# Kernel optimization log

Measured on AMD Instinct MI355X. Metric: run time of the kernel, lower is better.

Reference implementation:

```python
import jax, jax.numpy as jnp
import numpy as np

N = 50000
E = 800000
T = 12
HID = 128
K = 3
F_IN = 7  # 1 (x) + 4 (env) + 2 (coords)
CIN = F_IN + HID  # DCRNN concatenates input with hidden state


def setup_inputs() -> dict:
    key = jax.random.key(0)
    ks = jax.random.split(key, 16)
    inp = {
        "x": jax.random.normal(ks[0], (N, T), dtype=jnp.float32),
        "env": jax.random.normal(ks[1], (N, 4, T), dtype=jnp.float32),
        "coords": jax.random.uniform(ks[2], (N, 2), dtype=jnp.float32),
        "edge_index": jax.random.randint(ks[3], (2, E), 0, N, dtype=jnp.int32),
        "edge_weight": jax.random.uniform(ks[4], (E,), dtype=jnp.float32),
        "local_night": jax.random.uniform(ks[5], (N, T + 1), dtype=jnp.float32),
        # DCRNN gate diffusion-conv weights: [2 (out/in direction), K, Cin, Cout]
        "Wz": jax.random.normal(ks[6], (2, K, CIN, HID), dtype=jnp.float32) * 0.05,
        "bz": jnp.zeros((HID,), dtype=jnp.float32),
        "Wr": jax.random.normal(ks[7], (2, K, CIN, HID), dtype=jnp.float32) * 0.05,
        "br": jnp.zeros((HID,), dtype=jnp.float32),
        "Wh": jax.random.normal(ks[8], (2, K, CIN, HID), dtype=jnp.float32) * 0.05,
        "bh": jnp.zeros((HID,), dtype=jnp.float32),
        "lin_W": jax.random.normal(ks[9], (HID, 1), dtype=jnp.float32) * 0.05,
        "lin_b": jnp.zeros((1,), dtype=jnp.float32),
    }
    return inp


def reference(x, env, coords, edge_weight, local_night, Wz, bz, Wr, br, Wh, bh, lin_W, lin_b, edge_index):
    row, col = edge_index[0], edge_index[1]
    n = x.shape[0]

    # out/in degrees of the weighted adjacency A[row, col] = w
    deg_out = jax.ops.segment_sum(edge_weight, row, num_segments=n)
    deg_in = jax.ops.segment_sum(edge_weight, col, num_segments=n)
    inv_out = jnp.where(deg_out > 0, 1.0 / deg_out, 0.0)
    inv_in = jnp.where(deg_in > 0, 1.0 / deg_in, 0.0)

    def prop_out(v):  # (D_O^{-1} A) v : gather from col, scatter-add to row
        msg = edge_weight[:, None] * v[col]
        return inv_out[:, None] * jax.ops.segment_sum(msg, row, num_segments=n)

    def prop_in(v):  # (D_I^{-1} A^T) v : gather from row, scatter-add to col
        msg = edge_weight[:, None] * v[row]
        return inv_in[:, None] * jax.ops.segment_sum(msg, col, num_segments=n)

    def dconv(X, W, b):
        # K-hop bidirectional diffusion convolution
        H = X @ (W[0, 0] + W[1, 0])
        Tx0 = X
        Tx_o = prop_out(X)
        Tx_i = prop_in(X)
        H = H + Tx_o @ W[0, 1] + Tx_i @ W[1, 1]
        for k in range(2, W.shape[1]):
            Tx_o = 2.0 * prop_out(Tx_o) - Tx0
            Tx_i = 2.0 * prop_in(Tx_i) - Tx0
            H = H + Tx_o @ W[0, k] + Tx_i @ W[1, k]
        return H + b

    env_t = jnp.moveaxis(env, -1, 0)          # [T, N, 4]
    night_t = jnp.transpose(local_night[:, 1:])  # [T, N]
    hid0 = jnp.zeros((n, HID), dtype=x.dtype)   # hidden state resets each call (H=None)

    def step(x_prev, ts):
        e, night = ts
        X = jnp.concatenate([x_prev, e, coords], axis=1)   # [N, 7]
        Xh = jnp.concatenate([X, hid0], axis=1)            # [N, 7+HID]
        Z = jax.nn.sigmoid(dconv(Xh, Wz, bz))
        R = jax.nn.sigmoid(dconv(Xh, Wr, br))  # H*R = 0 since H0 = 0; kept for fidelity
        H_tilde = jnp.tanh(dconv(Xh, Wh, bh))
        H_new = Z * hid0 + (1.0 - Z) * H_tilde
        out = jax.nn.relu(H_new) @ lin_W + lin_b           # [N, 1]
        out = out * night[:, None]
        return out, out

    x0 = x[:, 0:1]
    _, preds = jax.lax.scan(step, x0, (env_t, night_t))    # preds: [T, N, 1]
    predictions = jnp.concatenate([x0, jnp.transpose(preds[..., 0])], axis=1)  # [N, T+1]
    return predictions
```

## Files before the change

kernel.cpp:

```cpp
#include <hip/hip_runtime.h>
#include <hip/hip_fp16.h>

#define Nn 50000
#define Ee 800000
#define Tt 12
#define NBAND 8
#define BAND 6250
#define CAP 64

__global__ __launch_bounds__(256) void csr_direct(
    const int* __restrict__ ei, const float* __restrict__ ew,
    int* __restrict__ nextR, int* __restrict__ nextC,
    unsigned* __restrict__ adjR, unsigned* __restrict__ adjC)
{
    int band = blockIdx.x & (NBAND - 1);
    int chunk = blockIdx.x >> 3;
    int lo = band * BAND, hi = lo + BAND;
    int stride = (gridDim.x >> 3) * 256;
    for (int e = chunk * 256 + threadIdx.x; e < Ee; e += stride) {
        int r = ei[e], c = ei[Ee + e];
        bool br = (r >= lo) & (r < hi);
        bool bc = (c >= lo) & (c < hi);
        if (br | bc) {
            unsigned wb = __half_as_ushort(__float2half(ew[e]));
            if (br) adjR[(r << 6) + atomicAdd(&nextR[r], 1)] = ((unsigned)c << 16) | wb;
            if (bc) adjC[(c << 6) + atomicAdd(&nextC[c], 1)] = ((unsigned)r << 16) | wb;
        }
    }
}

__global__ __launch_bounds__(256) void weff_kernel(
    const float* __restrict__ Wz, const float* __restrict__ Wh,
    const float* __restrict__ bz, const float* __restrict__ bh,
    float* __restrict__ wzT, float* __restrict__ whT)
{
    int idx = blockIdx.x * 256 + threadIdx.x;
    if (idx >= 2 * 36 * 128) return;
    const float* W = (idx < 36 * 128) ? Wz : Wh;
    const float* B = (idx < 36 * 128) ? bz : bh;
    float* O       = (idx < 36 * 128) ? wzT : whT;
    int rem = idx % (36 * 128);
    int k = rem / 128, j = rem % 128;
    float v;
    if (k == 35) v = B[j];
    else {
        int p = k / 7, rr = k % 7;
        if (p == 0)      v = W[(0 * 135 + rr) * 128 + j] + W[(3 * 135 + rr) * 128 + j];
        else if (p == 1) v = W[(1 * 135 + rr) * 128 + j];
        else if (p == 2) v = W[(4 * 135 + rr) * 128 + j];
        else if (p == 3) v = W[(2 * 135 + rr) * 128 + j];
        else             v = W[(5 * 135 + rr) * 128 + j];
    }
    O[k * 128 + j] = v;
}

__global__ __launch_bounds__(256) void initS_kernel(
    const float* __restrict__ x, const float* __restrict__ env,
    const float* __restrict__ coords,
    __half* __restrict__ S, __half* __restrict__ xcur, float* __restrict__ out)
{
    int i = blockIdx.x * 256 + threadIdx.x;
    if (i >= Nn) return;
    float xv = x[i * Tt];
    xcur[i] = __float2half(xv);
    out[i * 13] = xv;
    float4 ev[12];
    const float4* ep = (const float4*)(env + (long)i * 48);
    #pragma unroll
    for (int j = 0; j < 12; j++) ev[j] = ep[j];
    const float* evf = (const float*)ev;
    __half row[64];
    #pragma unroll
    for (int t = 0; t < 12; t++)
        #pragma unroll
        for (int c = 0; c < 4; c++)
            row[t * 4 + c] = __float2half(evf[c * 12 + t]);
    row[48] = __float2half(coords[i * 2]);
    row[49] = __float2half(coords[i * 2 + 1]);
    #pragma unroll
    for (int j = 50; j < 64; j++) row[j] = __half(0.f);
    uint4* dst = (uint4*)(S + (long)i * 64);
    const uint4* sv = (const uint4*)row;
    #pragma unroll
    for (int j = 0; j < 8; j++) dst[j] = sv[j];
}

__device__ __forceinline__ float wdec(unsigned ed) {
    return __half2float(__ushort_as_half((unsigned short)(ed & 0xffffu)));
}

__device__ __forceinline__ void acc8h(float* a, float w, uint4 hv) {
    float2 p0 = __half22float2(*(__half2*)&hv.x);
    float2 p1 = __half22float2(*(__half2*)&hv.y);
    float2 p2 = __half22float2(*(__half2*)&hv.z);
    float2 p3 = __half22float2(*(__half2*)&hv.w);
    a[0] = fmaf(w, p0.x, a[0]); a[1] = fmaf(w, p0.y, a[1]);
    a[2] = fmaf(w, p1.x, a[2]); a[3] = fmaf(w, p1.y, a[3]);
    a[4] = fmaf(w, p2.x, a[4]); a[5] = fmaf(w, p2.y, a[5]);
    a[6] = fmaf(w, p3.x, a[6]); a[7] = fmaf(w, p3.y, a[7]);
}

__device__ __forceinline__ void unpack8h(uint4 hv, float* f) {
    float2 p0 = __half22float2(*(__half2*)&hv.x);
    float2 p1 = __half22float2(*(__half2*)&hv.y);
    float2 p2 = __half22float2(*(__half2*)&hv.z);
    float2 p3 = __half22float2(*(__half2*)&hv.w);
    f[0] = p0.x; f[1] = p0.y; f[2] = p1.x; f[3] = p1.y;
    f[4] = p2.x; f[5] = p2.y; f[6] = p3.x; f[7] = p3.y;
}

__global__ __launch_bounds__(256) void prop_kernel(
    const int* __restrict__ cntR, const unsigned* __restrict__ adjR,
    const int* __restrict__ cntC, const unsigned* __restrict__ adjC,
    const __half* __restrict__ src_o, const __half* __restrict__ src_i,
    const __half* __restrict__ subS,
    __half* __restrict__ dst_o, __half* __restrict__ dst_i,
    float* __restrict__ inv_out, float* __restrict__ inv_in, int computeInv)
{
    int tid = blockIdx.x * 256 + threadIdx.x;
    if (tid >= Nn * 16) return;
    int team = tid >> 3;
    int node = team >> 1, dir = team & 1, s = tid & 7;
    const int*      cn  = dir ? cntC : cntR;
    const unsigned* adj = dir ? adjC : adjR;
    const __half*   src = dir ? src_i : src_o;
    __half*         dst = dir ? dst_i : dst_o;
    int b = node << 6, e = b + cn[node];
    float acc[8] = {0.f,0.f,0.f,0.f,0.f,0.f,0.f,0.f};
    float sw = 0.f;
    for (int k = b; k < e; k += 4) {
        bool v1 = k + 1 < e, v2 = k + 2 < e, v3 = k + 3 < e;
        unsigned e0 = adj[k];
        unsigned e1 = adj[v1 ? k + 1 : b];
        unsigned e2 = adj[v2 ? k + 2 : b];
        unsigned e3 = adj[v3 ? k + 3 : b];
        uint4 r0 = *(const uint4*)(src + (long)(e0 >> 16) * 64 + s * 8);
        uint4 r1 = *(const uint4*)(src + (long)(e1 >> 16) * 64 + s * 8);
        uint4 r2 = *(const uint4*)(src + (long)(e2 >> 16) * 64 + s * 8);
        uint4 r3 = *(const uint4*)(src + (long)(e3 >> 16) * 64 + s * 8);
        float w0 = wdec(e0);
        float w1 = v1 ? wdec(e1) : 0.f;
        float w2 = v2 ? wdec(e2) : 0.f;
        float w3 = v3 ? wdec(e3) : 0.f;
        acc8h(acc, w0, r0); acc8h(acc, w1, r1);
        acc8h(acc, w2, r2); acc8h(acc, w3, r3);
        sw += (w0 + w1) + (w2 + w3);
    }
    float inv;
    if (computeInv) {
        inv = sw > 0.f ? 1.f / sw : 0.f;
        if (s == 0) (dir ? inv_in : inv_out)[node] = inv;
    } else {
        inv = (dir ? inv_in : inv_out)[node];
    }
    float o8[8];
    if (subS) {
        uint4 sv4 = *(const uint4*)(subS + (long)node * 64 + s * 8);
        float sv[8];
        unpack8h(sv4, sv);
        #pragma unroll
        for (int q = 0; q < 8; q++) o8[q] = fmaf(2.f * inv, acc[q], -sv[q]);
    } else {
        #pragma unroll
        for (int q = 0; q < 8; q++) o8[q] = inv * acc[q];
    }
    __half2 h0 = __floats2half2_rn(o8[0], o8[1]);
    __half2 h1 = __floats2half2_rn(o8[2], o8[3]);
    __half2 h2 = __floats2half2_rn(o8[4], o8[5]);
    __half2 h3 = __floats2half2_rn(o8[6], o8[7]);
    uint4 st;
    st.x = *(unsigned*)&h0; st.y = *(unsigned*)&h1;
    st.z = *(unsigned*)&h2; st.w = *(unsigned*)&h3;
    *(uint4*)(dst + (long)node * 64 + s * 8) = st;
}

__global__ __launch_bounds__(256) void gx_kernel(
    const int* __restrict__ cntR, const unsigned* __restrict__ adjR,
    const int* __restrict__ cntC, const unsigned* __restrict__ adjC,
    const __half* __restrict__ xcur,
    __half* __restrict__ toX, __half* __restrict__ tiX,
    const float* __restrict__ inv_out, const float* __restrict__ inv_in)
{
    int tid = blockIdx.x * 256 + threadIdx.x;
    if (tid >= Nn * 8) return;
    int node = tid >> 3;
    int dir = (tid >> 2) & 1, sub = tid & 3;
    const int*      cn  = dir ? cntC : cntR;
    const unsigned* adj = dir ? adjC : adjR;
    int b = node << 6, e = b + cn[node];
    float acc = 0.f;
    int k0 = b + sub;
    {
        unsigned en[6]; bool v[6];
        #pragma unroll
        for (int s = 0; s < 6; s++) { int k = k0 + 4 * s; v[s] = k < e; en[s] = adj[v[s] ? k : b]; }
        __half xv[6];
        #pragma unroll
        for (int s = 0; s < 6; s++) xv[s] = xcur[v[s] ? (en[s] >> 16) : 0u];
        #pragma unroll
        for (int s = 0; s < 6; s++) acc += (v[s] ? wdec(en[s]) : 0.f) * __half2float(xv[s]);
        for (int k = k0 + 24; k < e; k += 4) {
            unsigned ed = adj[k];
            acc += wdec(ed) * __half2float(xcur[ed >> 16]);
        }
    }
    acc += __shfl_xor(acc, 1);
    acc += __shfl_xor(acc, 2);
    if (sub == 0) {
        float inv = (dir ? inv_in : inv_out)[node];
        (dir ? tiX : toX)[node] = __float2half(inv * acc);
    }
}

__global__ __launch_bounds__(256) void step_kernel(
    const int* __restrict__ cntR, const unsigned* __restrict__ adjR,
    const int* __restrict__ cntC, const unsigned* __restrict__ adjC,
    const float* __restrict__ inv_out, const float* __restrict__ inv_in,
    const float* __restrict__ env, const float* __restrict__ coords,
    const float* __restrict__ night,
    const float* __restrict__ wzT, const float* __restrict__ whT,
    const float* __restrict__ linW, const float* __restrict__ linb,
    __half* __restrict__ xcur,
    const __half* __restrict__ toX, const __half* __restrict__ tiX,
    const __half* __restrict__ P_o, const __half* __restrict__ P_i,
    const __half* __restrict__ P2_o, const __half* __restrict__ P2_i,
    float* __restrict__ out, int t)
{
    __shared__ float f_s[32][36];
    __shared__ float part_s[2][32];
    int tid = threadIdx.x;
    int base = blockIdx.x * 32;

    {
        int nl = tid >> 3;
        int dir = (tid >> 2) & 1, sub = tid & 3;
        int node = base + nl;
        int nc = node < Nn ? node : Nn - 1;
        const int*      cn  = dir ? cntC : cntR;
        const unsigned* adj = dir ? adjC : adjR;
        const __half*   src = dir ? tiX : toX;
        int b = nc << 6, e = b + cn[nc];
        float acc = 0.f;
        int k0 = b + sub;
        {
            unsigned en[6]; bool v[6];
            #pragma unroll
            for (int s = 0; s < 6; s++) { int k = k0 + 4 * s; v[s] = k < e; en[s] = adj[v[s] ? k : b]; }
            __half xv[6];
            #pragma unroll
            for (int s = 0; s < 6; s++) xv[s] = src[v[s] ? (en[s] >> 16) : 0u];
            #pragma unroll
            for (int s = 0; s < 6; s++) acc += (v[s] ? wdec(en[s]) : 0.f) * __half2float(xv[s]);
            for (int k = k0 + 24; k < e; k += 4) {
                unsigned ed = adj[k];
                acc += wdec(ed) * __half2float(src[ed >> 16]);
            }
        }
        acc += __shfl_xor(acc, 1);
        acc += __shfl_xor(acc, 2);
        if (sub == 0) {
            float inv = (dir ? inv_in : inv_out)[nc];
            float xval = __half2float(xcur[nc]);
            f_s[nl][21 + 7 * dir] = fmaf(2.f * inv, acc, -xval);
        }
    }
    {
        int g = tid >> 5;
        int n = tid & 31;
        int node = base + n;
        int nc = node < Nn ? node : Nn - 1;
        if (g == 0) {
            f_s[n][0] = __half2float(xcur[nc]);
            #pragma unroll
            for (int c = 0; c < 4; c++) f_s[n][1 + c] = env[(long)nc * 48 + c * 12 + t];
            f_s[n][5] = coords[nc * 2];
            f_s[n][6] = coords[nc * 2 + 1];
            f_s[n][35] = 1.f;
        } else if (g == 1) {
            f_s[n][7] = __half2float(toX[nc]);
            const __half* r = P_o + (long)nc * 64;
            #pragma unroll
            for (int c = 0; c < 4; c++) f_s[n][8 + c] = __half2float(r[t * 4 + c]);
            f_s[n][12] = __half2float(r[48]);
            f_s[n][13] = __half2float(r[49]);
        } else if (g == 2) {
            f_s[n][14] = __half2float(tiX[nc]);
            const __half* r = P_i + (long)nc * 64;
            #pragma unroll
            for (int c = 0; c < 4; c++) f_s[n][15 + c] = __half2float(r[t * 4 + c]);
            f_s[n][19] = __half2float(r[48]);
            f_s[n][20] = __half2float(r[49]);
        } else if (g == 3) {
            const __half* r = P2_o + (long)nc * 64;
            #pragma unroll
            for (int c = 0; c < 4; c++) f_s[n][22 + c] = __half2float(r[t * 4 + c]);
            f_s[n][26] = __half2float(r[48]);
            f_s[n][27] = __half2float(r[49]);
        } else if (g == 4) {
            const __half* r = P2_i + (long)nc * 64;
            #pragma unroll
            for (int c = 0; c < 4; c++) f_s[n][29 + c] = __half2float(r[t * 4 + c]);
            f_s[n][33] = __half2float(r[48]);
            f_s[n][34] = __half2float(r[49]);
        }
    }
    __syncthreads();

    int lane = tid & 63;
    int wave = tid >> 6;
    int chSel = wave & 1;
    int ch = chSel * 64 + lane;
    int half_id = wave >> 1;
    float wz[36], wh[36];
    #pragma unroll
    for (int k = 0; k < 36; k++) wz[k] = wzT[k * 128 + ch];
    #pragma unroll
    for (int k = 0; k < 36; k++) wh[k] = whT[k * 128 + ch];
    float lw = linW[ch];
    float lb = linb[0];

    #pragma unroll 1
    for (int n = 0; n < 16; n++) {
        int ni = half_id * 16 + n;
        const float4* fv = (const float4*)f_s[ni];
        float hz = 0.f, hh = 0.f;
        #pragma unroll
        for (int q = 0; q < 9; q++) {
            float4 fq = fv[q];
            hz = fmaf(fq.x, wz[q*4+0], hz); hh = fmaf(fq.x, wh[q*4+0], hh);
            hz = fmaf(fq.y, wz[q*4+1], hz); hh = fmaf(fq.y, wh[q*4+1], hh);
            hz = fmaf(fq.z, wz[q*4+2], hz); hh = fmaf(fq.z, wh[q*4+2], hh);
            hz = fmaf(fq.w, wz[q*4+3], hz); hh = fmaf(fq.w, wh[q*4+3], hh);
        }
        float z  = 1.f / (1.f + __expf(-hz));
        float e2 = __expf(2.f * hh);
        float ht = 1.f - 2.f / (e2 + 1.f);
        float v = fmaxf((1.f - z) * ht, 0.f) * lw;
        v += __shfl_xor(v, 1);  v += __shfl_xor(v, 2);  v += __shfl_xor(v, 4);
        v += __shfl_xor(v, 8);  v += __shfl_xor(v, 16); v += __shfl_xor(v, 32);
        if (lane == 0) part_s[chSel][ni] = v;
    }
    __syncthreads();
    if (tid < 32) {
        int node = base + tid;
        if (node < Nn) {
            float o = part_s[0][tid] + part_s[1][tid] + lb;
            o *= night[(long)node * 13 + t + 1];
            out[(long)node * 13 + t + 1] = o;
            if (t + 1 < Tt) xcur[node] = __float2half(o);
        }
    }
}

extern "C" void kernel_launch(void* const* d_in, const int* in_sizes, int n_in,
                              void* d_out, int out_size, void* d_ws, size_t ws_size,
                              hipStream_t stream) {
    const float* x      = (const float*)d_in[0];
    const float* env    = (const float*)d_in[1];
    const float* coords = (const float*)d_in[2];
    const int*   ei     = (const int*)d_in[3];
    const float* ew     = (const float*)d_in[4];
    const float* night  = (const float*)d_in[5];
    const float* Wz     = (const float*)d_in[6];
    const float* bz     = (const float*)d_in[7];
    const float* Wh     = (const float*)d_in[10];
    const float* bh     = (const float*)d_in[11];
    const float* linW   = (const float*)d_in[12];
    const float* linb   = (const float*)d_in[13];
    float* out = (float*)d_out;

    float* w = (float*)d_ws;
    float* wzT     = w;
    float* whT     = w + 4608;
    float* inv_out = w + 9216;
    float* inv_in  = w + 59216;
    __half* xcur   = (__half*)(w + 109216);
    __half* toX    = (__half*)(w + 134216);
    __half* tiX    = (__half*)(w + 159216);
    int* nextR     = (int*)(w + 184216);
    int* nextC     = (int*)(w + 234216);
    __half* S    = (__half*)(w + 284224);
    __half* P_o  = (__half*)(w + 1884224);
    __half* P_i  = (__half*)(w + 3484224);
    __half* P2_o = (__half*)(w + 5084224);
    __half* P2_i = (__half*)(w + 6684224);
    unsigned* adjR = (unsigned*)(w + 8284224);
    unsigned* adjC = (unsigned*)(w + 11484224);

    hipMemsetAsync(nextR, 0, 2 * Nn * sizeof(int), stream);
    csr_direct<<<8 * 256, 256, 0, stream>>>(ei, ew, nextR, nextC, adjR, adjC);

    weff_kernel<<<36, 256, 0, stream>>>(Wz, Wh, bz, bh, wzT, whT);
    initS_kernel<<<(Nn + 255) / 256, 256, 0, stream>>>(x, env, coords, S, xcur, out);

    prop_kernel<<<(Nn * 16) / 256, 256, 0, stream>>>(
        nextR, adjR, nextC, adjC, S, S, nullptr, P_o, P_i, inv_out, inv_in, 1);
    prop_kernel<<<(Nn * 16) / 256, 256, 0, stream>>>(
        nextR, adjR, nextC, adjC, P_o, P_i, S, P2_o, P2_i, inv_out, inv_in, 0);

    for (int t = 0; t < Tt; t++) {
        gx_kernel<<<(Nn * 8 + 255) / 256, 256, 0, stream>>>(
            nextR, adjR, nextC, adjC, xcur, toX, tiX, inv_out, inv_in);
        step_kernel<<<(Nn + 31) / 32, 256, 0, stream>>>(
            nextR, adjR, nextC, adjC, inv_out, inv_in,
            env, coords, night, wzT, whT, linW, linb,
            xcur, toX, tiX, P_o, P_i, P2_o, P2_i, out, t);
    }
}
```

Baseline: 719.6 us.

## Stage scalar node vector in LDS for per-step sparse propagations

Each time step's two scalar sparse propagations (gx and the second hop) now copy the whole 50000-entry half-precision source vector into shared memory (100 KB per block) and gather from LDS instead of global memory. The second-hop propagation moves out of the dense step kernel into its own t2_lds kernel, which writes float outputs that the dense kernel reads. This trades global random gathers for a per-block 100 KB bulk copy and one extra launch per step, and the large LDS footprint limits occupancy to one block per CU.

Measured after the change: 802.5 us. 11.5% more time.

```diff
diff --git a/kernel.cpp b/kernel.cpp
--- a/kernel.cpp
+++ b/kernel.cpp
@@ -7,6 +7,7 @@
 #define NBAND 8
 #define BAND 6250
 #define CAP 64
+#define NPB 196
 
 __global__ __launch_bounds__(256) void csr_direct(
     const int* __restrict__ ei, const float* __restrict__ ew,
@@ -174,54 +175,93 @@
     *(uint4*)(dst + (long)node * 64 + s * 8) = st;
 }
 
-__global__ __launch_bounds__(256) void gx_kernel(
+__global__ __launch_bounds__(1024) void gx_lds(
     const int* __restrict__ cntR, const unsigned* __restrict__ adjR,
     const int* __restrict__ cntC, const unsigned* __restrict__ adjC,
     const __half* __restrict__ xcur,
     __half* __restrict__ toX, __half* __restrict__ tiX,
     const float* __restrict__ inv_out, const float* __restrict__ inv_in)
 {
-    int tid = blockIdx.x * 256 + threadIdx.x;
-    if (tid >= Nn * 8) return;
-    int node = tid >> 3;
-    int dir = (tid >> 2) & 1, sub = tid & 3;
+    extern __shared__ __half xs[];
+    {
+        const uint4* s4 = (const uint4*)xcur;
+        uint4* d4 = (uint4*)xs;
+        for (int i = threadIdx.x; i < Nn / 8; i += 1024) d4[i] = s4[i];
+    }
+    __syncthreads();
+    int nbase = blockIdx.x * NPB;
+    int g = threadIdx.x >> 3, sub = threadIdx.x & 7;
+    for (int p = g; p < 2 * NPB; p += 128) {
+        int node = nbase + (p >> 1);
+        if (node >= Nn) continue;
+        int dir = p & 1;
+        const int*      cn  = dir ? cntC : cntR;
+        const unsigned* adj = dir ? adjC : adjR;
+        int b = node << 6, e = b + cn[node];
+        float acc = 0.f;
+        for (int k = b + sub; k < e; k += 8) {
+            unsigned ed = adj[k];
+            acc += wdec(ed) * __half2float(xs[ed >> 16]);
+        }
+        acc += __shfl_xor(acc, 1);
+        acc += __shfl_xor(acc, 2);
+        acc += __shfl_xor(acc, 4);
+        if (sub == 0) {
+            float inv = (dir ? inv_in : inv_out)[node];
+            (dir ? tiX : toX)[node] = __float2half(inv * acc);
+        }
+    }
+}
+
+__global__ __launch_bounds__(1024) void t2_lds(
+    const int* __restrict__ cntR, const unsigned* __restrict__ adjR,
+    const int* __restrict__ cntC, const unsigned* __restrict__ adjC,
+    const __half* __restrict__ toX, const __half* __restrict__ tiX,
+    const __half* __restrict__ xcur,
+    const float* __restrict__ inv_out, const float* __restrict__ inv_in,
+    float* __restrict__ t2o, float* __restrict__ t2i)
+{
+    extern __shared__ __half ss[];
+    int dir = blockIdx.x & 1;
+    int slice = blockIdx.x >> 1;
+    {
+        const uint4* s4 = (const uint4*)(dir ? tiX : toX);
+        uint4* d4 = (uint4*)ss;
+        for (int i = threadIdx.x; i < Nn / 8; i += 1024) d4[i] = s4[i];
+    }
+    __syncthreads();
     const int*      cn  = dir ? cntC : cntR;
     const unsigned* adj = dir ? adjC : adjR;
-    int b = node << 6, e = b + cn[node];
-    float acc = 0.f;
-    int k0 = b + sub;
-    {
-        unsigned en[6]; bool v[6];
-        #pragma unroll
-        for (int s = 0; s < 6; s++) { int k = k0 + 4 * s; v[s] = k < e; en[s] = adj[v[s] ? k : b]; }
-        __half xv[6];
-        #pragma unroll
-        for (int s = 0; s < 6; s++) xv[s] = xcur[v[s] ? (en[s] >> 16) : 0u];
-        #pragma unroll
-        for (int s = 0; s < 6; s++) acc += (v[s] ? wdec(en[s]) : 0.f) * __half2float(xv[s]);
-        for (int k = k0 + 24; k < e; k += 4) {
+    int nbase = slice * NPB;
+    int g = threadIdx.x >> 3, sub = threadIdx.x & 7;
+    for (int p = g; p < NPB; p += 128) {
+        int node = nbase + p;
+        if (node >= Nn) continue;
+        int b = node << 6, e = b + cn[node];
+        float acc = 0.f;
+        for (int k = b + sub; k < e; k += 8) {
             unsigned ed = adj[k];
-            acc += wdec(ed) * __half2float(xcur[ed >> 16]);
-        }
-    }
-    acc += __shfl_xor(acc, 1);
-    acc += __shfl_xor(acc, 2);
-    if (sub == 0) {
-        float inv = (dir ? inv_in : inv_out)[node];
-        (dir ? tiX : toX)[node] = __float2half(inv * acc);
-    }
-}
-
-__global__ __launch_bounds__(256) void step_kernel(
-    const int* __restrict__ cntR, const unsigned* __restrict__ adjR,
-    const int* __restrict__ cntC, const unsigned* __restrict__ adjC,
-    const float* __restrict__ inv_out, const float* __restrict__ inv_in,
+            acc += wdec(ed) * __half2float(ss[ed >> 16]);
+        }
+        acc += __shfl_xor(acc, 1);
+        acc += __shfl_xor(acc, 2);
+        acc += __shfl_xor(acc, 4);
+        if (sub == 0) {
+            float inv = (dir ? inv_in : inv_out)[node];
+            (dir ? t2i : t2o)[node] =
+                fmaf(2.f * inv, acc, -__half2float(xcur[node]));
+        }
+    }
+}
+
+__global__ __launch_bounds__(256) void dense_step(
     const float* __restrict__ env, const float* __restrict__ coords,
     const float* __restrict__ night,
     const float* __restrict__ wzT, const float* __restrict__ whT,
     const float* __restrict__ linW, const float* __restrict__ linb,
     __half* __restrict__ xcur,
     const __half* __restrict__ toX, const __half* __restrict__ tiX,
+    const float* __restrict__ t2o, const float* __restrict__ t2i,
     const __half* __restrict__ P_o, const __half* __restrict__ P_i,
     const __half* __restrict__ P2_o, const __half* __restrict__ P2_i,
     float* __restrict__ out, int t)
@@ -231,39 +271,6 @@
     int tid = threadIdx.x;
     int base = blockIdx.x * 32;
 
-    {
-        int nl = tid >> 3;
-        int dir = (tid >> 2) & 1, sub = tid & 3;
-        int node = base + nl;
-        int nc = node < Nn ? node : Nn - 1;
-        const int*      cn  = dir ? cntC : cntR;
-        const unsigned* adj = dir ? adjC : adjR;
-        const __half*   src = dir ? tiX : toX;
-        int b = nc << 6, e = b + cn[nc];
-        float acc = 0.f;
-        int k0 = b + sub;
-        {
-            unsigned en[6]; bool v[6];
-            #pragma unroll
-            for (int s = 0; s < 6; s++) { int k = k0 + 4 * s; v[s] = k < e; en[s] = adj[v[s] ? k : b]; }
-            __half xv[6];
-            #pragma unroll
-            for (int s = 0; s < 6; s++) xv[s] = src[v[s] ? (en[s] >> 16) : 0u];
-            #pragma unroll
-            for (int s = 0; s < 6; s++) acc += (v[s] ? wdec(en[s]) : 0.f) * __half2float(xv[s]);
-            for (int k = k0 + 24; k < e; k += 4) {
-                unsigned ed = adj[k];
-                acc += wdec(ed) * __half2float(src[ed >> 16]);
-            }
-        }
-        acc += __shfl_xor(acc, 1);
-        acc += __shfl_xor(acc, 2);
-        if (sub == 0) {
-            float inv = (dir ? inv_in : inv_out)[nc];
-            float xval = __half2float(xcur[nc]);
-            f_s[nl][21 + 7 * dir] = fmaf(2.f * inv, acc, -xval);
-        }
-    }
     {
         int g = tid >> 5;
         int n = tid & 31;
@@ -291,12 +298,14 @@
             f_s[n][19] = __half2float(r[48]);
             f_s[n][20] = __half2float(r[49]);
         } else if (g == 3) {
+            f_s[n][21] = t2o[nc];
             const __half* r = P2_o + (long)nc * 64;
             #pragma unroll
             for (int c = 0; c < 4; c++) f_s[n][22 + c] = __half2float(r[t * 4 + c]);
             f_s[n][26] = __half2float(r[48]);
             f_s[n][27] = __half2float(r[49]);
         } else if (g == 4) {
+            f_s[n][28] = t2i[nc];
             const __half* r = P2_i + (long)nc * 64;
             #pragma unroll
             for (int c = 0; c < 4; c++) f_s[n][29 + c] = __half2float(r[t * 4 + c]);
@@ -377,15 +386,26 @@
     __half* xcur   = (__half*)(w + 109216);
     __half* toX    = (__half*)(w + 134216);
     __half* tiX    = (__half*)(w + 159216);
-    int* nextR     = (int*)(w + 184216);
-    int* nextC     = (int*)(w + 234216);
-    __half* S    = (__half*)(w + 284224);
-    __half* P_o  = (__half*)(w + 1884224);
-    __half* P_i  = (__half*)(w + 3484224);
-    __half* P2_o = (__half*)(w + 5084224);
-    __half* P2_i = (__half*)(w + 6684224);
-    unsigned* adjR = (unsigned*)(w + 8284224);
-    unsigned* adjC = (unsigned*)(w + 11484224);
+    float* t2o     = w + 184216;
+    float* t2i     = w + 234216;
+    int* nextR     = (int*)(w + 284216);
+    int* nextC     = (int*)(w + 334216);
+    __half* S    = (__half*)(w + 384224);
+    __half* P_o  = (__half*)(w + 1984224);
+    __half* P_i  = (__half*)(w + 3584224);
+    __half* P2_o = (__half*)(w + 5184224);
+    __half* P2_i = (__half*)(w + 6784224);
+    unsigned* adjR = (unsigned*)(w + 8384224);
+    unsigned* adjC = (unsigned*)(w + 11584224);
+
+    static bool attrSet = false;
+    if (!attrSet) {
+        hipFuncSetAttribute((const void*)gx_lds,
+            hipFuncAttributeMaxDynamicSharedMemorySize, Nn * 2);
+        hipFuncSetAttribute((const void*)t2_lds,
+            hipFuncAttributeMaxDynamicSharedMemorySize, Nn * 2);
+        attrSet = true;
+    }
 
     hipMemsetAsync(nextR, 0, 2 * Nn * sizeof(int), stream);
     csr_direct<<<8 * 256, 256, 0, stream>>>(ei, ew, nextR, nextC, adjR, adjC);
@@ -399,11 +419,12 @@
         nextR, adjR, nextC, adjC, P_o, P_i, S, P2_o, P2_i, inv_out, inv_in, 0);
 
     for (int t = 0; t < Tt; t++) {
-        gx_kernel<<<(Nn * 8 + 255) / 256, 256, 0, stream>>>(
+        gx_lds<<<256, 1024, Nn * 2, stream>>>(
             nextR, adjR, nextC, adjC, xcur, toX, tiX, inv_out, inv_in);
-        step_kernel<<<(Nn + 31) / 32, 256, 0, stream>>>(
-            nextR, adjR, nextC, adjC, inv_out, inv_in,
+        t2_lds<<<512, 1024, Nn * 2, stream>>>(
+            nextR, adjR, nextC, adjC, toX, tiX, xcur, inv_out, inv_in, t2o, t2i);
+        dense_step<<<(Nn + 31) / 32, 256, 0, stream>>>(
             env, coords, night, wzT, whT, linW, linb,
-            xcur, toX, tiX, P_o, P_i, P2_o, P2_i, out, t);
-    }
-}
+            xcur, toX, tiX, t2o, t2i, P_o, P_i, P2_o, P2_i, out, t);
+    }
+}
```
